# Kernel tuning notes

Measured on AMD Instinct MI355X. Metric: run time of the kernel, lower is better.

The kernel has to match this reference:

```python
import jax, jax.numpy as jnp
import numpy as np

# ---- static config (matches init_kwargs) ----
IN_DIM = 1024
HIDDEN = 4096
U_OUT = 4
PROJ = HIDDEN // U_OUT          # 1024
BS = 64                          # block_size
NB = IN_DIM // BS                # 16 blocks (in == mid == out padded dims)
NRE = 3                          # n_reuploads
RANK = 64
EPS = 1e-5

# fixed stride permutation: arange.view(NB,BS).t().reshape(-1); mid_dim == in_padded so no pad/repeat
PERM = np.arange(NB * BS).reshape(NB, BS).T.reshape(-1)  # [1024]


def setup_inputs() -> dict:
    key = jax.random.key(0)
    ks = jax.random.split(key, 12)
    x = jax.random.normal(ks[0], (4, 2048, IN_DIM), dtype=jnp.float32)
    R = jax.random.normal(ks[1], (NB, BS, BS), dtype=jnp.float32) / jnp.sqrt(BS * 1.0)
    L = jax.random.normal(ks[2], (NB, BS, BS), dtype=jnp.float32) / jnp.sqrt(BS * 1.0)
    bias = jnp.zeros((PROJ,), jnp.float32)
    gamma = jnp.ones((PROJ,), jnp.float32)
    beta = jnp.zeros((PROJ,), jnp.float32)
    Wd = jax.random.normal(ks[3], (PROJ, RANK), dtype=jnp.float32) * 0.01   # down: dim->rank
    Wu = jax.random.normal(ks[4], (RANK, PROJ), dtype=jnp.float32) * 0.01   # up: rank->dim (torch init=0; nonzero for grad coverage)
    thetas = jnp.ones((NRE, PROJ), jnp.float32) + 0.1 * jax.random.normal(ks[5], (NRE, PROJ), dtype=jnp.float32)
    phis = 0.1 * jax.random.normal(ks[6], (NRE, PROJ), dtype=jnp.float32)
    Wp = jax.random.normal(ks[7], (U_OUT, 2 * NRE), dtype=jnp.float32) / jnp.sqrt(2.0 * NRE)
    bp = jnp.zeros((U_OUT,), jnp.float32)
    return {"x": x, "R": R, "L": L, "bias": bias, "gamma": gamma, "beta": beta,
            "Wd": Wd, "Wu": Wu, "thetas": thetas, "phis": phis, "Wp": Wp, "bp": bp}


def reference(x, R, L, bias, gamma, beta, Wd, Wu, thetas, phis, Wp, bp):
    B, S, _ = x.shape
    N = B * S
    # ---- MonarchProj: block-diag R, stride permute, block-diag L ----
    h = x.reshape(N, NB, BS)
    h = jnp.einsum('nbi,bij->nbj', h, R).reshape(N, NB * BS)
    h = h[:, PERM].reshape(N, NB, BS)
    h = jnp.einsum('nbi,bij->nbj', h, L).reshape(N, NB * BS)
    h = (h + bias).reshape(B, S, PROJ)
    # ---- LayerNorm ----
    mu = h.mean(-1, keepdims=True)
    var = ((h - mu) ** 2).mean(-1, keepdims=True)
    h = (h - mu) * jax.lax.rsqrt(var + EPS) * gamma + beta
    # ---- low-rank entangle: x + up(down(x)) ----
    h = h + (h @ Wd) @ Wu
    # ---- per-reupload rotation, interleaved sin/cos stacked on last dim ----
    rot = h[..., None] * thetas.T + phis.T                    # [B,S,PROJ,NRE]
    sc = jnp.stack([jnp.sin(rot), jnp.cos(rot)], axis=-1)     # [B,S,PROJ,NRE,2]
    sc = sc.reshape(B, S, PROJ, 2 * NRE)                      # [s0,c0,s1,c1,s2,c2]
    # ---- tiny final Linear then flatten ----
    out = sc @ Wp.T + bp                                      # [B,S,PROJ,U_OUT]
    return out.reshape(B, S, HIDDEN)
```

## Files before the change

### kernel.cpp

```cpp
#include <hip/hip_runtime.h>


typedef __attribute__((ext_vector_type(8))) short bf16x8;
typedef __attribute__((ext_vector_type(4))) float f32x4;

#define PITCH 1032
#define DPITCH 68
#define DHALF (16 * DPITCH)
#define SMEM_BYTES 59392
#undef SMEM_BYTES
#define SMEM_BYTES 75904

__device__ __forceinline__ unsigned short f2bf(float f) {
    unsigned u = __float_as_uint(f);
    u = (u + 0x7FFFu + ((u >> 16) & 1u)) >> 16;
    return (unsigned short)u;
}
__device__ __forceinline__ float bf2f(unsigned short h) {
    return __uint_as_float(((unsigned)h) << 16);
}
__device__ __forceinline__ unsigned cvt_pk_bf16(float a, float b) {
    unsigned r;
    asm("v_cvt_pk_bf16_f32 %0, %1, %2" : "=v"(r) : "v"(a), "v"(b));
    return r;
}
__device__ __forceinline__ void split2(float a, float b, unsigned &H, unsigned &L) {
    H = cvt_pk_bf16(a, b);
    const float ha = __uint_as_float(H << 16);
    const float hb = __uint_as_float(H & 0xFFFF0000u);
    L = cvt_pk_bf16(a - ha, b - hb);
}
__device__ __forceinline__ f32x4 MFMA(bf16x8 a, bf16x8 b, f32x4 c) {
    return __builtin_amdgcn_mfma_f32_16x16x32_bf16(a, b, c, 0, 0, 0);
}
__device__ __forceinline__ f32x4 ntload4(const float* p) {
    return __builtin_nontemporal_load((const f32x4*)p);
}
__device__ __forceinline__ void ntstore4(float* p, f32x4 v) {
    __builtin_nontemporal_store(v, (f32x4*)p);
}

__global__ __launch_bounds__(256) void pack_weights(
    const float* __restrict__ R, const float* __restrict__ L,
    const float* __restrict__ Wd, const float* __restrict__ Wu,
    const float* __restrict__ gamma, const float* __restrict__ beta,
    const float* __restrict__ thetas, const float* __restrict__ phis,
    unsigned short* __restrict__ wsp)
{
    const int bx = blockIdx.x;
    const int tid = threadIdx.x;
    if (bx == 64) {
        float* bc = (float*)(wsp + (size_t)64 * 8192);
        const float INV2PI = 0.15915494309189535f;
        for (int i = tid; i < 1024; i += 256) {
            float* t = bc + 128 + i * 8;
            t[0] = gamma[i];                 t[1] = beta[i];
            t[2] = thetas[i] * INV2PI;       t[3] = thetas[1024 + i] * INV2PI;
            t[4] = thetas[2048 + i] * INV2PI;
            t[5] = phis[i] * INV2PI;         t[6] = phis[1024 + i] * INV2PI;
            t[7] = phis[2048 + i] * INV2PI;
        }
        __shared__ float red[8][64];
        const int r = tid & 63, part = tid >> 6;
        float sb = 0.f, sc = 0.f;
        for (int c = part * 256; c < part * 256 + 256; ++c) {
            const float w = Wd[(size_t)c * 64 + r];
            sb += gamma[c] * w;
            sc += beta[c] * w;
        }
        red[part][r] = sb; red[part + 4][r] = sc;
        __syncthreads();
        if (part == 0) {
            bc[r]      = red[0][r] + red[1][r] + red[2][r] + red[3][r];
            bc[64 + r] = red[4][r] + red[5][r] + red[6][r] + red[7][r];
        }
        return;
    }
    const int blk = bx;
    __shared__ float M[4096];
    if (blk < 16) {
        const float* src = R + (size_t)blk * 4096;
        #pragma unroll
        for (int t = tid * 4; t < 4096; t += 1024)
            *(float4*)&M[t] = *(const float4*)&src[t];
    } else if (blk < 32) {
        const float* src = L + (size_t)(blk - 16) * 4096;
        #pragma unroll
        for (int t = tid * 4; t < 4096; t += 1024)
            *(float4*)&M[t] = *(const float4*)&src[t];
    } else if (blk < 48) {
        const float* src = Wd + (size_t)(blk - 32) * 4096;
        const float* gsrc = gamma + (blk - 32) * 64;
        #pragma unroll
        for (int t = tid * 4; t < 4096; t += 1024) {
            const float gm = gsrc[t >> 6];
            float4 wv = *(const float4*)&src[t];
            wv.x *= gm; wv.y *= gm; wv.z *= gm; wv.w *= gm;
            *(float4*)&M[t] = wv;
        }
    } else {
        const float* src = Wu + (blk - 48) * 64;
        #pragma unroll
        for (int t = tid * 4; t < 4096; t += 1024) {
            const int k = t >> 6, j = t & 63;
            *(float4*)&M[t] = *(const float4*)&src[(size_t)k * 1024 + j];
        }
    }
    __syncthreads();
    unsigned short* dst = wsp + (size_t)blk * 8192;
    for (int it = 0; it < 4; ++it) {
        const int slot = tid + it * 256;
        const int fragidx = slot >> 6;
        const int l = slot & 63;
        const int kk = fragidx >> 3;
        const int nt = (fragidx >> 1) & 3;
        const int comp = fragidx & 1;
        const int g = l >> 4, r16 = l & 15;
        const int j = nt * 16 + r16;
        bf16x8 s;
        #pragma unroll
        for (int v = 0; v < 8; ++v) {
            const int k = kk * 32 + g * 8 + v;
            const float w = M[k * 64 + j];
            unsigned short hi = f2bf(w);
            unsigned short bits = (comp == 0) ? hi : f2bf(w - bf2f(hi));
            s[v] = (short)bits;
        }
        *(bf16x8*)(dst + fragidx * 512 + l * 8) = s;
    }
}

__global__ __launch_bounds__(512, 4) void qrun_main(
    const float* __restrict__ x, const float* __restrict__ bias,
    const float* __restrict__ Wp, const float* __restrict__ bpv,
    const unsigned short* __restrict__ wpk, float* __restrict__ out)
{
    extern __shared__ char smem[];
    unsigned short* hiP = (unsigned short*)smem;
    unsigned short* loP = hiP + 16 * PITCH;
    float* dbuf = (float*)(loP + 16 * PITCH);
    float* lnpart = dbuf + 2 * DHALF;
    float* statsR = lnpart + 256;

    const int tid = threadIdx.x;
    const int wave = tid >> 6, lane = tid & 63;
    const int g = lane >> 4, r16 = lane & 15;
    const int grp = wave >> 2, ntw = wave & 3;
    const size_t n0 = (size_t)blockIdx.x * 16;
    const int rowA = r16 * PITCH;

    {
        const float* xb = x + n0 * 1024;
        #pragma unroll
        for (int it = 0; it < 4; ++it) {
            const int base = (it * 512 + tid) * 8;
            const int row = base >> 10, col = base & 1023;
            const f32x4 f0 = ntload4(xb + base);
            const f32x4 f1 = ntload4(xb + base + 4);
            unsigned H0, L0, H1, L1, H2, L2, H3, L3;
            split2(f0[0], f0[1], H0, L0);
            split2(f0[2], f0[3], H1, L1);
            split2(f1[0], f1[1], H2, L2);
            split2(f1[2], f1[3], H3, L3);
            *(uint4*)(hiP + row * PITCH + col) = make_uint4(H0, H1, H2, H3);
            *(uint4*)(loP + row * PITCH + col) = make_uint4(L0, L1, L2, L3);
        }
    }
    __syncthreads();

    f32x4 acc1[8];
    #pragma unroll
    for (int bi = 0; bi < 8; ++bi) {
        const int b = grp * 8 + bi;
        const unsigned short* wb = wpk + (size_t)b * 8192;
        bf16x8 Bh0 = *(const bf16x8*)(wb + ((0*4+ntw)*2+0)*512 + lane*8);
        bf16x8 Bh1 = *(const bf16x8*)(wb + ((1*4+ntw)*2+0)*512 + lane*8);
        const int ca = b * 64 + g * 8;
        bf16x8 Ah0 = *(const bf16x8*)(hiP + rowA + ca);
        bf16x8 Al0 = *(const bf16x8*)(loP + rowA + ca);
        bf16x8 Ah1 = *(const bf16x8*)(hiP + rowA + ca + 32);
        bf16x8 Al1 = *(const bf16x8*)(loP + rowA + ca + 32);
        f32x4 a = {0.f, 0.f, 0.f, 0.f};
        a = MFMA(Ah0, Bh0, a); a = MFMA(Al0, Bh0, a);
        a = MFMA(Ah1, Bh1, a); a = MFMA(Al1, Bh1, a);
        acc1[bi] = a;
    }
    __syncthreads();

    {
        const int Cw = (ntw * 4 + (r16 >> 2)) * 64 + ((r16 >> 1) & 1) * 32
                     + (((grp + 2 * (r16 & 1)) ^ (r16 >> 2)) << 3);
        #pragma unroll
        for (int v = 0; v < 4; ++v) {
            const int rowv = (g * 4 + v) * PITCH;
            unsigned h0, l0, h1, l1, h2, l2, h3, l3;
            split2(acc1[0][v], acc1[1][v], h0, l0);
            split2(acc1[2][v], acc1[3][v], h1, l1);
            split2(acc1[4][v], acc1[5][v], h2, l2);
            split2(acc1[6][v], acc1[7][v], h3, l3);
            *(uint4*)(hiP + rowv + Cw) = make_uint4(h0, h1, h2, h3);
            *(uint4*)(loP + rowv + Cw) = make_uint4(l0, l1, l2, l3);
        }
    }
    __syncthreads();

    f32x4 acc2[8];
    #pragma unroll
    for (int ci = 0; ci < 8; ++ci) {
        const int c = grp * 8 + ci;
        const unsigned short* wb = wpk + (size_t)(16 + c) * 8192;
        bf16x8 Wh0 = *(const bf16x8*)(wb + ((0*4+ntw)*2+0)*512 + lane*8);
        bf16x8 Wh1 = *(const bf16x8*)(wb + ((1*4+ntw)*2+0)*512 + lane*8);
        const int gx = ((g ^ (c & 3)) << 3);
        const int c0 = rowA + c * 64 + gx;
        bf16x8 Hh0 = *(const bf16x8*)(hiP + c0);
        bf16x8 Hl0 = *(const bf16x8*)(loP + c0);
        bf16x8 Hh1 = *(const bf16x8*)(hiP + c0 + 32);
        bf16x8 Hl1 = *(const bf16x8*)(loP + c0 + 32);
        f32x4 a = {0.f, 0.f, 0.f, 0.f};
        a = MFMA(Wh0, Hh0, a); a = MFMA(Wh0, Hl0, a);
        a = MFMA(Wh1, Hh1, a); a = MFMA(Wh1, Hl1, a);
        acc2[ci] = a;
    }
    __syncthreads();

    {
        float s = 0.f, s2 = 0.f;
        #pragma unroll
        for (int ci = 0; ci < 8; ++ci) {
            const int c = grp * 8 + ci;
            const int ncol = c * 64 + ntw * 16 + g * 4;
            const float4 bv = *(const float4*)(bias + ncol);
            const float f0 = acc2[ci][0] + bv.x;
            const float f1 = acc2[ci][1] + bv.y;
            const float f2 = acc2[ci][2] + bv.z;
            const float f3 = acc2[ci][3] + bv.w;
            s += f0 + f1 + f2 + f3;
            s2 += f0 * f0 + f1 * f1 + f2 * f2 + f3 * f3;
            unsigned hA, lA, hB, lB;
            split2(f0, f1, hA, lA);
            split2(f2, f3, hB, lB);
            *(uint2*)(hiP + rowA + ncol) = make_uint2(hA, hB);
            *(uint2*)(loP + rowA + ncol) = make_uint2(lA, lB);
        }
        s  += __shfl_xor(s, 16);  s  += __shfl_xor(s, 32);
        s2 += __shfl_xor(s2, 16); s2 += __shfl_xor(s2, 32);
        if (g == 0) {
            lnpart[(wave * 16 + r16) * 2]     = s;
            lnpart[(wave * 16 + r16) * 2 + 1] = s2;
        }
    }
    __syncthreads();

    if (tid < 16) {
        float s = 0.f, s2 = 0.f;
        #pragma unroll
        for (int w = 0; w < 8; ++w) {
            s  += lnpart[(w * 16 + tid) * 2];
            s2 += lnpart[(w * 16 + tid) * 2 + 1];
        }
        const float mu = s * (1.f / 1024.f);
        statsR[tid * 2]     = mu;
        statsR[tid * 2 + 1] = rsqrtf(s2 * (1.f / 1024.f) - mu * mu + 1e-5f);
    }
    {
        f32x4 accd = {0.f, 0.f, 0.f, 0.f};
        #pragma unroll
        for (int ki = 0; ki < 16; ++ki) {
            const int kq = grp * 16 + ki;
            const int kb = kq >> 1, kin = kq & 1;
            const unsigned short* wb = wpk + (size_t)(32 + kb) * 8192;
            bf16x8 Wh = *(const bf16x8*)(wb + ((kin*4+ntw)*2+0)*512 + lane*8);
            bf16x8 Hh = *(const bf16x8*)(hiP + rowA + kq * 32 + g * 8);
            accd = MFMA(Wh, Hh, accd);
        }
        *(f32x4*)(dbuf + grp * DHALF + r16 * DPITCH + ntw * 16 + g * 4) = accd;
    }
    __syncthreads();

    const float* bcf = (const float*)(wpk + (size_t)64 * 8192);
    const float muT = statsR[r16 * 2], rsT = statsR[r16 * 2 + 1];
    float muR[4], rsR[4];
    #pragma unroll
    for (int v = 0; v < 4; ++v) {
        muR[v] = statsR[(g * 4 + v) * 2];
        rsR[v] = statsR[(g * 4 + v) * 2 + 1];
    }
    bf16x8 dA[2];
    #pragma unroll
    for (int kk = 0; kk < 2; ++kk) {
        const int rb = kk * 32 + g * 8;
        const float4 B0 = *(const float4*)(bcf + rb);
        const float4 B1 = *(const float4*)(bcf + rb + 4);
        const float4 C0 = *(const float4*)(bcf + 64 + rb);
        const float4 C1 = *(const float4*)(bcf + 64 + rb + 4);
        const float Ba[8] = {B0.x,B0.y,B0.z,B0.w,B1.x,B1.y,B1.z,B1.w};
        const float Ca[8] = {C0.x,C0.y,C0.z,C0.w,C1.x,C1.y,C1.z,C1.w};
        const int di = r16 * DPITCH + rb;
        const f32x4 q0 = *(const f32x4*)(dbuf + di);
        const f32x4 q1 = *(const f32x4*)(dbuf + di + 4);
        const f32x4 p0 = *(const f32x4*)(dbuf + DHALF + di);
        const f32x4 p1 = *(const f32x4*)(dbuf + DHALF + di + 4);
        float dv[8];
        #pragma unroll
        for (int v = 0; v < 4; ++v) {
            dv[v]     = rsT * (q0[v] + p0[v]) - muT * rsT * Ba[v]     + Ca[v];
            dv[v + 4] = rsT * (q1[v] + p1[v]) - muT * rsT * Ba[v + 4] + Ca[v + 4];
        }
        const uint4 uu = make_uint4(cvt_pk_bf16(dv[0], dv[1]),
                                    cvt_pk_bf16(dv[2], dv[3]),
                                    cvt_pk_bf16(dv[4], dv[5]),
                                    cvt_pk_bf16(dv[6], dv[7]));
        dA[kk] = __builtin_bit_cast(bf16x8, uu);
    }
    float wp[24];
    #pragma unroll
    for (int k2 = 0; k2 < 24; ++k2) wp[k2] = Wp[k2];
    const float bp0 = bpv[0], bp1 = bpv[1], bp2 = bpv[2], bp3 = bpv[3];

    #pragma unroll 1
    for (int j = 0; j < 8; ++j) {
        const int ntg = wave * 8 + j;
        const int nb = ntg >> 2, ntin = ntg & 3;
        const unsigned short* wb = wpk + (size_t)(48 + nb) * 8192;
        bf16x8 Bh0 = *(const bf16x8*)(wb + ((0*4+ntin)*2+0)*512 + lane*8);
        bf16x8 Bh1 = *(const bf16x8*)(wb + ((1*4+ntin)*2+0)*512 + lane*8);
        f32x4 au = {0.f, 0.f, 0.f, 0.f};
        au = MFMA(dA[0], Bh0, au);
        au = MFMA(dA[1], Bh1, au);
        const int p = ntg * 16 + r16;
        const float4 t0 = *(const float4*)(bcf + 128 + p * 8);
        const float4 t1 = *(const float4*)(bcf + 128 + p * 8 + 4);
        const float gp = t0.x, bpp = t0.y;
        const float th0 = t0.z, th1 = t0.w, th2 = t1.x;
        const float ph0 = t1.y, ph1 = t1.z, ph2 = t1.w;
        #pragma unroll
        for (int v = 0; v < 4; ++v) {
            const int row = g * 4 + v;
            const float hraw = bf2f(hiP[row * PITCH + p]) + bf2f(loP[row * PITCH + p]);
            const float hn = (hraw - muR[v]) * rsR[v] * gp + bpp;
            const float e = au[v] + hn;
            float o0 = bp0, o1 = bp1, o2 = bp2, o3 = bp3;
            float arg, sn, cs;
            asm("v_fract_f32 %0, %1" : "=v"(arg) : "v"(fmaf(e, th0, ph0)));
            asm("v_sin_f32 %0, %1" : "=v"(sn) : "v"(arg));
            asm("v_cos_f32 %0, %1" : "=v"(cs) : "v"(arg));
            o0 = fmaf(sn, wp[0],  fmaf(cs, wp[1],  o0));
            o1 = fmaf(sn, wp[6],  fmaf(cs, wp[7],  o1));
            o2 = fmaf(sn, wp[12], fmaf(cs, wp[13], o2));
            o3 = fmaf(sn, wp[18], fmaf(cs, wp[19], o3));
            asm("v_fract_f32 %0, %1" : "=v"(arg) : "v"(fmaf(e, th1, ph1)));
            asm("v_sin_f32 %0, %1" : "=v"(sn) : "v"(arg));
            asm("v_cos_f32 %0, %1" : "=v"(cs) : "v"(arg));
            o0 = fmaf(sn, wp[2],  fmaf(cs, wp[3],  o0));
            o1 = fmaf(sn, wp[8],  fmaf(cs, wp[9],  o1));
            o2 = fmaf(sn, wp[14], fmaf(cs, wp[15], o2));
            o3 = fmaf(sn, wp[20], fmaf(cs, wp[21], o3));
            asm("v_fract_f32 %0, %1" : "=v"(arg) : "v"(fmaf(e, th2, ph2)));
            asm("v_sin_f32 %0, %1" : "=v"(sn) : "v"(arg));
            asm("v_cos_f32 %0, %1" : "=v"(cs) : "v"(arg));
            o0 = fmaf(sn, wp[4],  fmaf(cs, wp[5],  o0));
            o1 = fmaf(sn, wp[10], fmaf(cs, wp[11], o1));
            o2 = fmaf(sn, wp[16], fmaf(cs, wp[17], o2));
            o3 = fmaf(sn, wp[22], fmaf(cs, wp[23], o3));
            f32x4 ov = {o0, o1, o2, o3};
            ntstore4(out + ((n0 + row) * 1024 + p) * 4, ov);
        }
    }
}

extern "C" void kernel_launch(void* const* d_in, const int* in_sizes, int n_in,
                              void* d_out, int out_size, void* d_ws, size_t ws_size,
                              hipStream_t stream) {
    const float* x      = (const float*)d_in[0];
    const float* R      = (const float*)d_in[1];
    const float* L      = (const float*)d_in[2];
    const float* bias   = (const float*)d_in[3];
    const float* gamma  = (const float*)d_in[4];
    const float* beta   = (const float*)d_in[5];
    const float* Wd     = (const float*)d_in[6];
    const float* Wu     = (const float*)d_in[7];
    const float* thetas = (const float*)d_in[8];
    const float* phis   = (const float*)d_in[9];
    const float* Wp     = (const float*)d_in[10];
    const float* bp     = (const float*)d_in[11];
    float* out = (float*)d_out;
    unsigned short* wsp = (unsigned short*)d_ws;
    const int N = in_sizes[0] / 1024;

    (void)hipFuncSetAttribute((const void*)qrun_main,
                              hipFuncAttributeMaxDynamicSharedMemorySize, SMEM_BYTES);
    pack_weights<<<dim3(65), dim3(256), 0, stream>>>(R, L, Wd, Wu, gamma, beta,
                                                     thetas, phis, wsp);
    qrun_main<<<dim3(N / 16), dim3(512), SMEM_BYTES, stream>>>(
        x, bias, Wp, bp, wsp, out);
}
```

Measured before the change: 52.57 us.

## Replace split bf16 hi/lo planes with single fp16 plane and MFMA

Switches the activation and weight representation from a two-term bf16 hi/lo split to a single fp16 value, which halves the MFMA count in the Monarch stages and removes the lo shared-memory plane. Shared memory per block shrinks, so the launch-bounds occupancy hint rises from 4 to 6. The Wp/bp loads are also made wave-uniform via readfirstlane. The cost is lower accuracy: fp16 has fewer mantissa bits than the bf16 hi+lo pair and a narrower exponent range, which may break tolerance.

```diff
diff --git a/kernel.cpp b/kernel.cpp
--- a/kernel.cpp
+++ b/kernel.cpp
@@ -1,37 +1,20 @@
 #include <hip/hip_runtime.h>
 
 
-typedef __attribute__((ext_vector_type(8))) short bf16x8;
+typedef __attribute__((ext_vector_type(8))) _Float16 f16x8;
+typedef __attribute__((ext_vector_type(4))) _Float16 f16x4;
 typedef __attribute__((ext_vector_type(4))) float f32x4;
 
 #define PITCH 1032
 #define DPITCH 68
 #define DHALF (16 * DPITCH)
-#define SMEM_BYTES 59392
-#undef SMEM_BYTES
-#define SMEM_BYTES 75904
-
-__device__ __forceinline__ unsigned short f2bf(float f) {
-    unsigned u = __float_as_uint(f);
-    u = (u + 0x7FFFu + ((u >> 16) & 1u)) >> 16;
-    return (unsigned short)u;
-}
-__device__ __forceinline__ float bf2f(unsigned short h) {
-    return __uint_as_float(((unsigned)h) << 16);
-}
-__device__ __forceinline__ unsigned cvt_pk_bf16(float a, float b) {
-    unsigned r;
-    asm("v_cvt_pk_bf16_f32 %0, %1, %2" : "=v"(r) : "v"(a), "v"(b));
-    return r;
-}
-__device__ __forceinline__ void split2(float a, float b, unsigned &H, unsigned &L) {
-    H = cvt_pk_bf16(a, b);
-    const float ha = __uint_as_float(H << 16);
-    const float hb = __uint_as_float(H & 0xFFFF0000u);
-    L = cvt_pk_bf16(a - ha, b - hb);
-}
-__device__ __forceinline__ f32x4 MFMA(bf16x8 a, bf16x8 b, f32x4 c) {
-    return __builtin_amdgcn_mfma_f32_16x16x32_bf16(a, b, c, 0, 0, 0);
+#define SMEM_BYTES 42880
+
+__device__ __forceinline__ f32x4 MFMA16(f16x8 a, f16x8 b, f32x4 c) {
+    return __builtin_amdgcn_mfma_f32_16x16x32_f16(a, b, c, 0, 0, 0);
+}
+__device__ __forceinline__ float uniformf(float f) {
+    return __uint_as_float(__builtin_amdgcn_readfirstlane(__float_as_uint(f)));
 }
 __device__ __forceinline__ f32x4 ntload4(const float* p) {
     return __builtin_nontemporal_load((const f32x4*)p);
@@ -117,30 +100,27 @@
         const int comp = fragidx & 1;
         const int g = l >> 4, r16 = l & 15;
         const int j = nt * 16 + r16;
-        bf16x8 s;
+        f16x8 s;
         #pragma unroll
         for (int v = 0; v < 8; ++v) {
             const int k = kk * 32 + g * 8 + v;
             const float w = M[k * 64 + j];
-            unsigned short hi = f2bf(w);
-            unsigned short bits = (comp == 0) ? hi : f2bf(w - bf2f(hi));
-            s[v] = (short)bits;
-        }
-        *(bf16x8*)(dst + fragidx * 512 + l * 8) = s;
-    }
-}
-
-__global__ __launch_bounds__(512, 4) void qrun_main(
+            s[v] = (comp == 0) ? (_Float16)w : (_Float16)0.f;
+        }
+        *(uint4*)(dst + fragidx * 512 + l * 8) = __builtin_bit_cast(uint4, s);
+    }
+}
+
+__global__ __launch_bounds__(512, 6) void qrun_main(
     const float* __restrict__ x, const float* __restrict__ bias,
     const float* __restrict__ Wp, const float* __restrict__ bpv,
     const unsigned short* __restrict__ wpk, float* __restrict__ out)
 {
     extern __shared__ char smem[];
-    unsigned short* hiP = (unsigned short*)smem;
-    unsigned short* loP = hiP + 16 * PITCH;
-    float* dbuf = (float*)(loP + 16 * PITCH);
-    float* lnpart = dbuf + 2 * DHALF;
-    float* statsR = lnpart + 256;
+    unsigned short* plane = (unsigned short*)smem;
+    float* dbuf = (float*)(smem + 33024);
+    float* lnpart = (float*)(smem + 41728);
+    float* statsR = (float*)(smem + 42752);
 
     const int tid = threadIdx.x;
     const int wave = tid >> 6, lane = tid & 63;
@@ -157,13 +137,12 @@
             const int row = base >> 10, col = base & 1023;
             const f32x4 f0 = ntload4(xb + base);
             const f32x4 f1 = ntload4(xb + base + 4);
-            unsigned H0, L0, H1, L1, H2, L2, H3, L3;
-            split2(f0[0], f0[1], H0, L0);
-            split2(f0[2], f0[3], H1, L1);
-            split2(f1[0], f1[1], H2, L2);
-            split2(f1[2], f1[3], H3, L3);
-            *(uint4*)(hiP + row * PITCH + col) = make_uint4(H0, H1, H2, H3);
-            *(uint4*)(loP + row * PITCH + col) = make_uint4(L0, L1, L2, L3);
+            f16x8 hv;
+            hv[0] = (_Float16)f0[0]; hv[1] = (_Float16)f0[1];
+            hv[2] = (_Float16)f0[2]; hv[3] = (_Float16)f0[3];
+            hv[4] = (_Float16)f1[0]; hv[5] = (_Float16)f1[1];
+            hv[6] = (_Float16)f1[2]; hv[7] = (_Float16)f1[3];
+            *(uint4*)(plane + row * PITCH + col) = __builtin_bit_cast(uint4, hv);
         }
     }
     __syncthreads();
@@ -173,16 +152,14 @@
     for (int bi = 0; bi < 8; ++bi) {
         const int b = grp * 8 + bi;
         const unsigned short* wb = wpk + (size_t)b * 8192;
-        bf16x8 Bh0 = *(const bf16x8*)(wb + ((0*4+ntw)*2+0)*512 + lane*8);
-        bf16x8 Bh1 = *(const bf16x8*)(wb + ((1*4+ntw)*2+0)*512 + lane*8);
+        f16x8 Bh0 = *(const f16x8*)(wb + ((0*4+ntw)*2+0)*512 + lane*8);
+        f16x8 Bh1 = *(const f16x8*)(wb + ((1*4+ntw)*2+0)*512 + lane*8);
         const int ca = b * 64 + g * 8;
-        bf16x8 Ah0 = *(const bf16x8*)(hiP + rowA + ca);
-        bf16x8 Al0 = *(const bf16x8*)(loP + rowA + ca);
-        bf16x8 Ah1 = *(const bf16x8*)(hiP + rowA + ca + 32);
-        bf16x8 Al1 = *(const bf16x8*)(loP + rowA + ca + 32);
+        f16x8 Ah0 = *(const f16x8*)(plane + rowA + ca);
+        f16x8 Ah1 = *(const f16x8*)(plane + rowA + ca + 32);
         f32x4 a = {0.f, 0.f, 0.f, 0.f};
-        a = MFMA(Ah0, Bh0, a); a = MFMA(Al0, Bh0, a);
-        a = MFMA(Ah1, Bh1, a); a = MFMA(Al1, Bh1, a);
+        a = MFMA16(Ah0, Bh0, a);
+        a = MFMA16(Ah1, Bh1, a);
         acc1[bi] = a;
     }
     __syncthreads();
@@ -193,13 +170,12 @@
         #pragma unroll
         for (int v = 0; v < 4; ++v) {
             const int rowv = (g * 4 + v) * PITCH;
-            unsigned h0, l0, h1, l1, h2, l2, h3, l3;
-            split2(acc1[0][v], acc1[1][v], h0, l0);
-            split2(acc1[2][v], acc1[3][v], h1, l1);
-            split2(acc1[4][v], acc1[5][v], h2, l2);
-            split2(acc1[6][v], acc1[7][v], h3, l3);
-            *(uint4*)(hiP + rowv + Cw) = make_uint4(h0, h1, h2, h3);
-            *(uint4*)(loP + rowv + Cw) = make_uint4(l0, l1, l2, l3);
+            f16x8 hv;
+            hv[0] = (_Float16)acc1[0][v]; hv[1] = (_Float16)acc1[1][v];
+            hv[2] = (_Float16)acc1[2][v]; hv[3] = (_Float16)acc1[3][v];
+            hv[4] = (_Float16)acc1[4][v]; hv[5] = (_Float16)acc1[5][v];
+            hv[6] = (_Float16)acc1[6][v]; hv[7] = (_Float16)acc1[7][v];
+            *(uint4*)(plane + rowv + Cw) = __builtin_bit_cast(uint4, hv);
         }
     }
     __syncthreads();
@@ -209,17 +185,15 @@
     for (int ci = 0; ci < 8; ++ci) {
         const int c = grp * 8 + ci;
         const unsigned short* wb = wpk + (size_t)(16 + c) * 8192;
-        bf16x8 Wh0 = *(const bf16x8*)(wb + ((0*4+ntw)*2+0)*512 + lane*8);
-        bf16x8 Wh1 = *(const bf16x8*)(wb + ((1*4+ntw)*2+0)*512 + lane*8);
+        f16x8 Wh0 = *(const f16x8*)(wb + ((0*4+ntw)*2+0)*512 + lane*8);
+        f16x8 Wh1 = *(const f16x8*)(wb + ((1*4+ntw)*2+0)*512 + lane*8);
         const int gx = ((g ^ (c & 3)) << 3);
         const int c0 = rowA + c * 64 + gx;
-        bf16x8 Hh0 = *(const bf16x8*)(hiP + c0);
-        bf16x8 Hl0 = *(const bf16x8*)(loP + c0);
-        bf16x8 Hh1 = *(const bf16x8*)(hiP + c0 + 32);
-        bf16x8 Hl1 = *(const bf16x8*)(loP + c0 + 32);
+        f16x8 Hh0 = *(const f16x8*)(plane + c0);
+        f16x8 Hh1 = *(const f16x8*)(plane + c0 + 32);
         f32x4 a = {0.f, 0.f, 0.f, 0.f};
-        a = MFMA(Wh0, Hh0, a); a = MFMA(Wh0, Hl0, a);
-        a = MFMA(Wh1, Hh1, a); a = MFMA(Wh1, Hl1, a);
+        a = MFMA16(Wh0, Hh0, a);
+        a = MFMA16(Wh1, Hh1, a);
         acc2[ci] = a;
     }
     __syncthreads();
@@ -237,11 +211,10 @@
             const float f3 = acc2[ci][3] + bv.w;
             s += f0 + f1 + f2 + f3;
             s2 += f0 * f0 + f1 * f1 + f2 * f2 + f3 * f3;
-            unsigned hA, lA, hB, lB;
-            split2(f0, f1, hA, lA);
-            split2(f2, f3, hB, lB);
-            *(uint2*)(hiP + rowA + ncol) = make_uint2(hA, hB);
-            *(uint2*)(loP + rowA + ncol) = make_uint2(lA, lB);
+            f16x4 hq;
+            hq[0] = (_Float16)f0; hq[1] = (_Float16)f1;
+            hq[2] = (_Float16)f2; hq[3] = (_Float16)f3;
+            *(uint2*)(plane + rowA + ncol) = __builtin_bit_cast(uint2, hq);
         }
         s  += __shfl_xor(s, 16);  s  += __shfl_xor(s, 32);
         s2 += __shfl_xor(s2, 16); s2 += __shfl_xor(s2, 32);
@@ -270,9 +243,9 @@
             const int kq = grp * 16 + ki;
             const int kb = kq >> 1, kin = kq & 1;
             const unsigned short* wb = wpk + (size_t)(32 + kb) * 8192;
-            bf16x8 Wh = *(const bf16x8*)(wb + ((kin*4+ntw)*2+0)*512 + lane*8);
-            bf16x8 Hh = *(const bf16x8*)(hiP + rowA + kq * 32 + g * 8);
-            accd = MFMA(Wh, Hh, accd);
+            f16x8 Wh = *(const f16x8*)(wb + ((kin*4+ntw)*2+0)*512 + lane*8);
+            f16x8 Hh = *(const f16x8*)(plane + rowA + kq * 32 + g * 8);
+            accd = MFMA16(Wh, Hh, accd);
         }
         *(f32x4*)(dbuf + grp * DHALF + r16 * DPITCH + ntw * 16 + g * 4) = accd;
     }
@@ -286,7 +259,7 @@
         muR[v] = statsR[(g * 4 + v) * 2];
         rsR[v] = statsR[(g * 4 + v) * 2 + 1];
     }
-    bf16x8 dA[2];
+    f16x8 dA[2];
     #pragma unroll
     for (int kk = 0; kk < 2; ++kk) {
         const int rb = kk * 32 + g * 8;
@@ -301,33 +274,30 @@
         const f32x4 q1 = *(const f32x4*)(dbuf + di + 4);
         const f32x4 p0 = *(const f32x4*)(dbuf + DHALF + di);
         const f32x4 p1 = *(const f32x4*)(dbuf + DHALF + di + 4);
-        float dv[8];
+        f16x8 dq;
         #pragma unroll
         for (int v = 0; v < 4; ++v) {
-            dv[v]     = rsT * (q0[v] + p0[v]) - muT * rsT * Ba[v]     + Ca[v];
-            dv[v + 4] = rsT * (q1[v] + p1[v]) - muT * rsT * Ba[v + 4] + Ca[v + 4];
-        }
-        const uint4 uu = make_uint4(cvt_pk_bf16(dv[0], dv[1]),
-                                    cvt_pk_bf16(dv[2], dv[3]),
-                                    cvt_pk_bf16(dv[4], dv[5]),
-                                    cvt_pk_bf16(dv[6], dv[7]));
-        dA[kk] = __builtin_bit_cast(bf16x8, uu);
+            dq[v]     = (_Float16)(rsT * (q0[v] + p0[v]) - muT * rsT * Ba[v]     + Ca[v]);
+            dq[v + 4] = (_Float16)(rsT * (q1[v] + p1[v]) - muT * rsT * Ba[v + 4] + Ca[v + 4]);
+        }
+        dA[kk] = dq;
     }
     float wp[24];
     #pragma unroll
-    for (int k2 = 0; k2 < 24; ++k2) wp[k2] = Wp[k2];
-    const float bp0 = bpv[0], bp1 = bpv[1], bp2 = bpv[2], bp3 = bpv[3];
+    for (int k2 = 0; k2 < 24; ++k2) wp[k2] = uniformf(Wp[k2]);
+    const float bp0 = uniformf(bpv[0]), bp1 = uniformf(bpv[1]);
+    const float bp2 = uniformf(bpv[2]), bp3 = uniformf(bpv[3]);
 
     #pragma unroll 1
     for (int j = 0; j < 8; ++j) {
         const int ntg = wave * 8 + j;
         const int nb = ntg >> 2, ntin = ntg & 3;
         const unsigned short* wb = wpk + (size_t)(48 + nb) * 8192;
-        bf16x8 Bh0 = *(const bf16x8*)(wb + ((0*4+ntin)*2+0)*512 + lane*8);
-        bf16x8 Bh1 = *(const bf16x8*)(wb + ((1*4+ntin)*2+0)*512 + lane*8);
+        f16x8 Bh0 = *(const f16x8*)(wb + ((0*4+ntin)*2+0)*512 + lane*8);
+        f16x8 Bh1 = *(const f16x8*)(wb + ((1*4+ntin)*2+0)*512 + lane*8);
         f32x4 au = {0.f, 0.f, 0.f, 0.f};
-        au = MFMA(dA[0], Bh0, au);
-        au = MFMA(dA[1], Bh1, au);
+        au = MFMA16(dA[0], Bh0, au);
+        au = MFMA16(dA[1], Bh1, au);
         const int p = ntg * 16 + r16;
         const float4 t0 = *(const float4*)(bcf + 128 + p * 8);
         const float4 t1 = *(const float4*)(bcf + 128 + p * 8 + 4);
@@ -337,7 +307,7 @@
         #pragma unroll
         for (int v = 0; v < 4; ++v) {
             const int row = g * 4 + v;
-            const float hraw = bf2f(hiP[row * PITCH + p]) + bf2f(loP[row * PITCH + p]);
+            const float hraw = (float)*(const _Float16*)(plane + row * PITCH + p);
             const float hn = (hraw - muR[v]) * rsR[v] * gp + bpp;
             const float e = au[v] + hn;
             float o0 = bp0, o1 = bp1, o2 = bp2, o3 = bp3;
```

New measurement: 50.75 us. 3.5% less time.
